# Performance work log

Measured on AMD Instinct MI355X. Metric: run time of the kernel, lower is better.

Reference implementation:

```python
import jax, jax.numpy as jnp
import numpy as np

B, N, H = 128, 512, 512
NEG_INF = -1e30


def setup_inputs() -> dict:
    key = jax.random.key(0)
    k1, k2, k3, k4 = jax.random.split(key, 4)
    code_feat = jax.random.normal(k1, (B, N, H), dtype=jnp.float32)
    node_mask = jax.random.randint(k2, (B, N), 0, 2, dtype=jnp.int32)
    node_mask = node_mask.at[:, 0].set(1)  # ensure >=1 valid node per sample
    scale = 1.0 / np.sqrt(H)
    W_sa = jax.random.normal(k3, (H, H), dtype=jnp.float32) * scale
    b_sa = jnp.zeros((H,), dtype=jnp.float32)
    w_sc = jax.random.normal(k4, (H,), dtype=jnp.float32) * scale
    b_sc = jnp.zeros((), dtype=jnp.float32)
    return {"code_feat": code_feat, "node_mask": node_mask,
            "W_sa": W_sa, "b_sa": b_sa, "w_sc": w_sc, "b_sc": b_sc}


def reference(code_feat, node_mask, W_sa, b_sa, w_sc, b_sc):
    # code_sa_tanh = self_atten_scalar(tanh(self_atten(code_feat)))  -> [B, N]
    h = jnp.tanh(jnp.einsum('bnh,hk->bnk', code_feat, W_sa) + b_sa)
    scores = jnp.einsum('bnk,k->bn', h, w_sc) + b_sc  # [B, N]
    valid = node_mask.astype(bool)
    # masked_select + softmax over selected nodes == masked softmax; invalid
    # positions get weight 0, so the weighted sum over all nodes matches the
    # original per-sample bmm over the ragged selection exactly.
    scores = jnp.where(valid, scores, NEG_INF)
    attn = jax.nn.softmax(scores, axis=1)  # [B, N]
    pooled = jnp.einsum('bn,bnh->bh', attn, code_feat)  # [B, H]
    return jnp.tanh(pooled)
```

## Files before the change

kernel.cpp:

```cpp
#include <hip/hip_runtime.h>

#define NEG_INF (-1e30f)

typedef __bf16 bf16x8 __attribute__((ext_vector_type(8)));
typedef float  f32x4  __attribute__((ext_vector_type(4)));
typedef unsigned short ushort;

__device__ inline ushort f2bf(float f) {
    union { float f; unsigned u; } v; v.f = f;
    unsigned r = v.u + 0x7fffu + ((v.u >> 16) & 1u);
    return (ushort)(r >> 16);
}

__device__ inline float fast_tanhf(float x) {
    return 1.0f - 2.0f / (1.0f + __expf(2.0f * x));
}

__global__ void convw_kernel(const float* __restrict__ W, ushort* __restrict__ Wt) {
    int i = blockIdx.x * 256 + threadIdx.x;
    int h = i >> 9, c = i & 511;
    Wt[c * 512 + h] = f2bf(W[i]);
}

__global__ __launch_bounds__(512) void gemm_scores_kernel(
    const float* __restrict__ feat, const ushort* __restrict__ Wt,
    const float* __restrict__ b_sa, const float* __restrict__ w_sc,
    const float* __restrict__ b_sc, const int* __restrict__ mask,
    float* __restrict__ scores) {

    __shared__ ushort Alds[64 * 40];
    __shared__ ushort Blds[512 * 40];
    __shared__ float  wpart[8][64];

    const int tid  = threadIdx.x;
    const int m0   = blockIdx.x * 64;
    const int lane = tid & 63;
    const int wv   = tid >> 6;
    const int lr   = lane & 15;
    const int lk   = (lane >> 4) * 8;

    f32x4 acc[4][4];
#pragma unroll
    for (int a = 0; a < 4; ++a)
#pragma unroll
        for (int bn = 0; bn < 4; ++bn)
            acc[a][bn] = (f32x4){0.f, 0.f, 0.f, 0.f};

    const int arow = tid >> 3;
    const int acol = (tid & 7) * 4;
    const int brow = tid >> 2;
    const int bcol = (tid & 3) * 8;

    for (int k0 = 0; k0 < 512; k0 += 32) {
        __syncthreads();
        {
            const float4 v = *reinterpret_cast<const float4*>(
                feat + (size_t)(m0 + arow) * 512 + k0 + acol);
            ushort4 bv;
            bv.x = f2bf(v.x); bv.y = f2bf(v.y); bv.z = f2bf(v.z); bv.w = f2bf(v.w);
            *reinterpret_cast<ushort4*>(&Alds[arow * 40 + acol]) = bv;
        }
#pragma unroll
        for (int it = 0; it < 4; ++it) {
            int c = it * 128 + brow;
            uint4 raw = *reinterpret_cast<const uint4*>(Wt + (size_t)c * 512 + k0 + bcol);
            *reinterpret_cast<uint4*>(&Blds[c * 40 + bcol]) = raw;
        }
        __syncthreads();

        bf16x8 af[4], bfv[4];
#pragma unroll
        for (int a = 0; a < 4; ++a)
            af[a] = *reinterpret_cast<const bf16x8*>(&Alds[(a * 16 + lr) * 40 + lk]);
#pragma unroll
        for (int bn = 0; bn < 4; ++bn)
            bfv[bn] = *reinterpret_cast<const bf16x8*>(&Blds[(wv * 64 + bn * 16 + lr) * 40 + lk]);
#pragma unroll
        for (int a = 0; a < 4; ++a)
#pragma unroll
            for (int bn = 0; bn < 4; ++bn)
                acc[a][bn] = __builtin_amdgcn_mfma_f32_16x16x32_bf16(
                    af[a], bfv[bn], acc[a][bn], 0, 0, 0);
    }

    float rsum[4][4];
#pragma unroll
    for (int a = 0; a < 4; ++a)
#pragma unroll
        for (int r = 0; r < 4; ++r) rsum[a][r] = 0.0f;

#pragma unroll
    for (int bn = 0; bn < 4; ++bn) {
        int c = wv * 64 + bn * 16 + lr;
        float wsc = w_sc[c];
        float bsa = b_sa[c];
#pragma unroll
        for (int a = 0; a < 4; ++a)
#pragma unroll
            for (int r = 0; r < 4; ++r)
                rsum[a][r] += fast_tanhf(acc[a][bn][r] + bsa) * wsc;
    }
#pragma unroll
    for (int a = 0; a < 4; ++a)
#pragma unroll
        for (int r = 0; r < 4; ++r) {
            float v = rsum[a][r];
            v += __shfl_xor(v, 1);
            v += __shfl_xor(v, 2);
            v += __shfl_xor(v, 4);
            v += __shfl_xor(v, 8);
            rsum[a][r] = v;
        }
    if (lr == 0) {
        int rg = lane >> 4;
#pragma unroll
        for (int a = 0; a < 4; ++a)
#pragma unroll
            for (int r = 0; r < 4; ++r)
                wpart[wv][a * 16 + rg * 4 + r] = rsum[a][r];
    }
    __syncthreads();
    if (tid < 64) {
        float s = b_sc[0];
#pragma unroll
        for (int w2 = 0; w2 < 8; ++w2) s += wpart[w2][tid];
        int m = m0 + tid;
        scores[m] = mask[m] ? s : NEG_INF;
    }
}

__global__ void softmax_kernel(float* __restrict__ scores) {
    int b = blockIdx.x, t = threadIdx.x;
    float s0 = scores[b * 512 + t];
    float s1 = scores[b * 512 + t + 256];
    float m = fmaxf(s0, s1);
#pragma unroll
    for (int o = 1; o < 64; o <<= 1) m = fmaxf(m, __shfl_xor(m, o));
    __shared__ float red[4];
    if ((t & 63) == 0) red[t >> 6] = m;
    __syncthreads();
    m = fmaxf(fmaxf(red[0], red[1]), fmaxf(red[2], red[3]));
    float e0 = __expf(s0 - m), e1 = __expf(s1 - m);
    float z = e0 + e1;
#pragma unroll
    for (int o = 1; o < 64; o <<= 1) z += __shfl_xor(z, o);
    __syncthreads();
    if ((t & 63) == 0) red[t >> 6] = z;
    __syncthreads();
    float inv = 1.0f / (red[0] + red[1] + red[2] + red[3]);
    scores[b * 512 + t]       = e0 * inv;
    scores[b * 512 + t + 256] = e1 * inv;
}

__global__ void pool_kernel(const float* __restrict__ feat,
                            const float* __restrict__ probs,
                            float* __restrict__ part) {
    int b = blockIdx.x, c = blockIdx.y, t = threadIdx.x;
    __shared__ float pl[64];
    if (t < 64) pl[t] = probs[b * 512 + c * 64 + t];
    __syncthreads();
    const float* fbase = feat + ((size_t)b * 512 + c * 64) * 512;
    float a0 = 0.f, a1 = 0.f;
#pragma unroll 8
    for (int n = 0; n < 64; ++n) {
        float p = pl[n];
        a0 = fmaf(p, fbase[(size_t)n * 512 + t], a0);
        a1 = fmaf(p, fbase[(size_t)n * 512 + t + 256], a1);
    }
    part[(size_t)c * 65536 + b * 512 + t]       = a0;
    part[(size_t)c * 65536 + b * 512 + t + 256] = a1;
}

__global__ void finish_kernel(const float* __restrict__ part, float* __restrict__ out) {
    int i = blockIdx.x * 256 + threadIdx.x;
    float s = 0.f;
#pragma unroll
    for (int c = 0; c < 8; ++c) s += part[(size_t)c * 65536 + i];
    out[i] = fast_tanhf(s);
}

extern "C" void kernel_launch(void* const* d_in, const int* in_sizes, int n_in,
                              void* d_out, int out_size, void* d_ws, size_t ws_size,
                              hipStream_t stream) {
    const float* feat = (const float*)d_in[0];
    const int*   mask = (const int*)d_in[1];
    const float* W_sa = (const float*)d_in[2];
    const float* b_sa = (const float*)d_in[3];
    const float* w_sc = (const float*)d_in[4];
    const float* b_sc = (const float*)d_in[5];
    float* out = (float*)d_out;

    char* ws = (char*)d_ws;
    ushort* Wt    = (ushort*)ws;
    float*  scores = (float*)(ws + 524288);
    float*  part   = (float*)(ws + 524288 + 262144);

    hipLaunchKernelGGL(convw_kernel, dim3(1024), dim3(256), 0, stream, W_sa, Wt);
    hipLaunchKernelGGL(gemm_scores_kernel, dim3(1024), dim3(512), 0, stream,
                       feat, Wt, b_sa, w_sc, b_sc, mask, scores);
    hipLaunchKernelGGL(softmax_kernel, dim3(128), dim3(256), 0, stream, scores);
    hipLaunchKernelGGL(pool_kernel, dim3(128, 8), dim3(256), 0, stream, feat, scores, part);
    hipLaunchKernelGGL(finish_kernel, dim3(256), dim3(256), 0, stream, part, out);
}
```

Before: 96.68 us.

## Retile score GEMM into 128x128 blocks with direct-to-LDS weight loads

The score GEMM moves from 64-row blocks covering all 512 output columns to 128x128 tiles on a 4x512 grid of 256-thread blocks. Weight tiles are copied straight into LDS with global_load_lds, and feature loads are issued before the barrier. Because each block now covers only part of the columns, partial row scores go to a workspace and the softmax kernel sums them and applies the mask and bias. The pool kernel switches to float4 loads over 128-node chunks with an LDS reduction, halving the partial outputs. The trade-off is that each feature tile is now read four times, once per column block, plus extra workspace traffic for the partial scores.

```diff
diff --git a/kernel.cpp b/kernel.cpp
--- a/kernel.cpp
+++ b/kernel.cpp
@@ -6,14 +6,20 @@
 typedef float  f32x4  __attribute__((ext_vector_type(4)));
 typedef unsigned short ushort;
 
-__device__ inline ushort f2bf(float f) {
+__device__ __forceinline__ float fast_tanhf(float x) {
+    return 1.0f - 2.0f / (1.0f + __expf(2.0f * x));
+}
+
+__device__ __forceinline__ ushort f2bf(float f) {
     union { float f; unsigned u; } v; v.f = f;
     unsigned r = v.u + 0x7fffu + ((v.u >> 16) & 1u);
     return (ushort)(r >> 16);
 }
 
-__device__ inline float fast_tanhf(float x) {
-    return 1.0f - 2.0f / (1.0f + __expf(2.0f * x));
+__device__ __forceinline__ void gload_lds16(const void* gsrc, void* ldsdst) {
+    __builtin_amdgcn_global_load_lds(
+        (const __attribute__((address_space(1))) unsigned int*)gsrc,
+        (__attribute__((address_space(3))) unsigned int*)ldsdst, 16, 0, 0);
 }
 
 __global__ void convw_kernel(const float* __restrict__ W, ushort* __restrict__ Wt) {
@@ -22,65 +28,75 @@
     Wt[c * 512 + h] = f2bf(W[i]);
 }
 
-__global__ __launch_bounds__(512) void gemm_scores_kernel(
+__global__ __launch_bounds__(256) void gemm_scores_kernel(
     const float* __restrict__ feat, const ushort* __restrict__ Wt,
     const float* __restrict__ b_sa, const float* __restrict__ w_sc,
-    const float* __restrict__ b_sc, const int* __restrict__ mask,
-    float* __restrict__ scores) {
-
-    __shared__ ushort Alds[64 * 40];
-    __shared__ ushort Blds[512 * 40];
-    __shared__ float  wpart[8][64];
+    float* __restrict__ sp) {
+
+    __shared__ ushort Alds[128 * 40];
+    __shared__ ushort Blds[128 * 32];
+    __shared__ float  redE[4][64];
 
     const int tid  = threadIdx.x;
-    const int m0   = blockIdx.x * 64;
+    const int by   = blockIdx.x;
+    const int m0   = blockIdx.y * 128;
+    const int n0   = by * 128;
     const int lane = tid & 63;
     const int wv   = tid >> 6;
+    const int wm   = wv >> 1, wn = wv & 1;
     const int lr   = lane & 15;
-    const int lk   = (lane >> 4) * 8;
+    const int kg   = lane >> 4;
+    const int lk   = kg * 8;
+
+    const int arow = tid >> 1;
+    const int aseg = (tid & 1) * 16;
+    const float* agp = feat + (size_t)(m0 + arow) * 512 + aseg;
 
     f32x4 acc[4][4];
 #pragma unroll
     for (int a = 0; a < 4; ++a)
 #pragma unroll
-        for (int bn = 0; bn < 4; ++bn)
-            acc[a][bn] = (f32x4){0.f, 0.f, 0.f, 0.f};
-
-    const int arow = tid >> 3;
-    const int acol = (tid & 7) * 4;
-    const int brow = tid >> 2;
-    const int bcol = (tid & 3) * 8;
+        for (int b = 0; b < 4; ++b) acc[a][b] = (f32x4){0.f, 0.f, 0.f, 0.f};
+
+    const int o1 = tid + 256;
+    const ushort* bg0 = Wt + (size_t)(n0 + (tid >> 2)) * 512 + (tid & 3) * 8;
+    const ushort* bg1 = Wt + (size_t)(n0 + (o1 >> 2)) * 512 + (o1 & 3) * 8;
 
     for (int k0 = 0; k0 < 512; k0 += 32) {
+        const float4 v0 = *reinterpret_cast<const float4*>(agp + k0);
+        const float4 v1 = *reinterpret_cast<const float4*>(agp + k0 + 4);
+        const float4 v2 = *reinterpret_cast<const float4*>(agp + k0 + 8);
+        const float4 v3 = *reinterpret_cast<const float4*>(agp + k0 + 12);
+
         __syncthreads();
-        {
-            const float4 v = *reinterpret_cast<const float4*>(
-                feat + (size_t)(m0 + arow) * 512 + k0 + acol);
-            ushort4 bv;
-            bv.x = f2bf(v.x); bv.y = f2bf(v.y); bv.z = f2bf(v.z); bv.w = f2bf(v.w);
-            *reinterpret_cast<ushort4*>(&Alds[arow * 40 + acol]) = bv;
-        }
-#pragma unroll
-        for (int it = 0; it < 4; ++it) {
-            int c = it * 128 + brow;
-            uint4 raw = *reinterpret_cast<const uint4*>(Wt + (size_t)c * 512 + k0 + bcol);
-            *reinterpret_cast<uint4*>(&Blds[c * 40 + bcol]) = raw;
-        }
+
+        gload_lds16(bg0 + k0, (char*)Blds + wv * 1024);
+        gload_lds16(bg1 + k0, (char*)Blds + 4096 + wv * 1024);
+
+        bf16x8 h0, h1;
+        h0[0] = (__bf16)v0.x; h0[1] = (__bf16)v0.y; h0[2] = (__bf16)v0.z; h0[3] = (__bf16)v0.w;
+        h0[4] = (__bf16)v1.x; h0[5] = (__bf16)v1.y; h0[6] = (__bf16)v1.z; h0[7] = (__bf16)v1.w;
+        h1[0] = (__bf16)v2.x; h1[1] = (__bf16)v2.y; h1[2] = (__bf16)v2.z; h1[3] = (__bf16)v2.w;
+        h1[4] = (__bf16)v3.x; h1[5] = (__bf16)v3.y; h1[6] = (__bf16)v3.z; h1[7] = (__bf16)v3.w;
+        *reinterpret_cast<bf16x8*>(&Alds[arow * 40 + aseg]) = h0;
+        *reinterpret_cast<bf16x8*>(&Alds[arow * 40 + aseg + 8]) = h1;
+
         __syncthreads();
 
         bf16x8 af[4], bfv[4];
 #pragma unroll
         for (int a = 0; a < 4; ++a)
-            af[a] = *reinterpret_cast<const bf16x8*>(&Alds[(a * 16 + lr) * 40 + lk]);
-#pragma unroll
-        for (int bn = 0; bn < 4; ++bn)
-            bfv[bn] = *reinterpret_cast<const bf16x8*>(&Blds[(wv * 64 + bn * 16 + lr) * 40 + lk]);
-#pragma unroll
-        for (int a = 0; a < 4; ++a)
-#pragma unroll
-            for (int bn = 0; bn < 4; ++bn)
-                acc[a][bn] = __builtin_amdgcn_mfma_f32_16x16x32_bf16(
-                    af[a], bfv[bn], acc[a][bn], 0, 0, 0);
+            af[a] = *reinterpret_cast<const bf16x8*>(
+                &Alds[(wm * 64 + a * 16 + lr) * 40 + lk]);
+#pragma unroll
+        for (int b = 0; b < 4; ++b)
+            bfv[b] = *reinterpret_cast<const bf16x8*>(&Blds[(wn * 64 + b * 16 + lr) * 32 + lk]);
+#pragma unroll
+        for (int a = 0; a < 4; ++a)
+#pragma unroll
+            for (int b = 0; b < 4; ++b)
+                acc[a][b] = __builtin_amdgcn_mfma_f32_16x16x32_bf16(
+                    af[a], bfv[b], acc[a][b], 0, 0, 0);
     }
 
     float rsum[4][4];
@@ -90,15 +106,15 @@
         for (int r = 0; r < 4; ++r) rsum[a][r] = 0.0f;
 
 #pragma unroll
-    for (int bn = 0; bn < 4; ++bn) {
-        int c = wv * 64 + bn * 16 + lr;
-        float wsc = w_sc[c];
-        float bsa = b_sa[c];
+    for (int b = 0; b < 4; ++b) {
+        int col = n0 + wn * 64 + b * 16 + lr;
+        float wsc = w_sc[col];
+        float bsa = b_sa[col];
 #pragma unroll
         for (int a = 0; a < 4; ++a)
 #pragma unroll
             for (int r = 0; r < 4; ++r)
-                rsum[a][r] += fast_tanhf(acc[a][bn][r] + bsa) * wsc;
+                rsum[a][r] += fast_tanhf(acc[a][b][r] + bsa) * wsc;
     }
 #pragma unroll
     for (int a = 0; a < 4; ++a)
@@ -112,27 +128,27 @@
             rsum[a][r] = v;
         }
     if (lr == 0) {
-        int rg = lane >> 4;
 #pragma unroll
         for (int a = 0; a < 4; ++a)
 #pragma unroll
             for (int r = 0; r < 4; ++r)
-                wpart[wv][a * 16 + rg * 4 + r] = rsum[a][r];
-    }
-    __syncthreads();
-    if (tid < 64) {
-        float s = b_sc[0];
-#pragma unroll
-        for (int w2 = 0; w2 < 8; ++w2) s += wpart[w2][tid];
-        int m = m0 + tid;
-        scores[m] = mask[m] ? s : NEG_INF;
-    }
-}
-
-__global__ void softmax_kernel(float* __restrict__ scores) {
+                redE[wv][a * 16 + kg * 4 + r] = rsum[a][r];
+    }
+    __syncthreads();
+    if (tid < 128) {
+        int wmo = tid >> 6, r64 = tid & 63;
+        sp[(size_t)by * 65536 + m0 + tid] = redE[wmo * 2][r64] + redE[wmo * 2 + 1][r64];
+    }
+}
+
+__global__ void softmax_kernel(const float* __restrict__ sp, const float* __restrict__ b_sc,
+                               const int* __restrict__ mask, float* __restrict__ probs) {
     int b = blockIdx.x, t = threadIdx.x;
-    float s0 = scores[b * 512 + t];
-    float s1 = scores[b * 512 + t + 256];
+    int i0 = b * 512 + t, i1 = i0 + 256;
+    float s0 = sp[i0] + sp[65536 + i0] + sp[131072 + i0] + sp[196608 + i0] + b_sc[0];
+    float s1 = sp[i1] + sp[65536 + i1] + sp[131072 + i1] + sp[196608 + i1] + b_sc[0];
+    if (!mask[i0]) s0 = NEG_INF;
+    if (!mask[i1]) s1 = NEG_INF;
     float m = fmaxf(s0, s1);
 #pragma unroll
     for (int o = 1; o < 64; o <<= 1) m = fmaxf(m, __shfl_xor(m, o));
@@ -148,34 +164,42 @@
     if ((t & 63) == 0) red[t >> 6] = z;
     __syncthreads();
     float inv = 1.0f / (red[0] + red[1] + red[2] + red[3]);
-    scores[b * 512 + t]       = e0 * inv;
-    scores[b * 512 + t + 256] = e1 * inv;
+    probs[i0] = e0 * inv;
+    probs[i1] = e1 * inv;
 }
 
 __global__ void pool_kernel(const float* __restrict__ feat,
                             const float* __restrict__ probs,
                             float* __restrict__ part) {
     int b = blockIdx.x, c = blockIdx.y, t = threadIdx.x;
-    __shared__ float pl[64];
-    if (t < 64) pl[t] = probs[b * 512 + c * 64 + t];
-    __syncthreads();
-    const float* fbase = feat + ((size_t)b * 512 + c * 64) * 512;
-    float a0 = 0.f, a1 = 0.f;
+    __shared__ float pl[128];
+    __shared__ float red2[2][512];
+    if (t < 128) pl[t] = probs[b * 512 + c * 128 + t];
+    __syncthreads();
+    int col4 = (t & 127) * 4;
+    int stripe = t >> 7;
+    const float* fb = feat + ((size_t)(b * 512 + c * 128 + stripe * 64)) * 512 + col4;
+    float4 a4 = {0.f, 0.f, 0.f, 0.f};
 #pragma unroll 8
     for (int n = 0; n < 64; ++n) {
-        float p = pl[n];
-        a0 = fmaf(p, fbase[(size_t)n * 512 + t], a0);
-        a1 = fmaf(p, fbase[(size_t)n * 512 + t + 256], a1);
-    }
-    part[(size_t)c * 65536 + b * 512 + t]       = a0;
-    part[(size_t)c * 65536 + b * 512 + t + 256] = a1;
+        float p = pl[stripe * 64 + n];
+        const float4 f4 = *reinterpret_cast<const float4*>(fb + (size_t)n * 512);
+        a4.x = fmaf(p, f4.x, a4.x);
+        a4.y = fmaf(p, f4.y, a4.y);
+        a4.z = fmaf(p, f4.z, a4.z);
+        a4.w = fmaf(p, f4.w, a4.w);
+    }
+    *reinterpret_cast<float4*>(&red2[stripe][col4]) = a4;
+    __syncthreads();
+    float x0 = red2[0][t] + red2[1][t];
+    float x1 = red2[0][t + 256] + red2[1][t + 256];
+    part[(size_t)c * 65536 + b * 512 + t]       = x0;
+    part[(size_t)c * 65536 + b * 512 + t + 256] = x1;
 }
 
 __global__ void finish_kernel(const float* __restrict__ part, float* __restrict__ out) {
     int i = blockIdx.x * 256 + threadIdx.x;
-    float s = 0.f;
-#pragma unroll
-    for (int c = 0; c < 8; ++c) s += part[(size_t)c * 65536 + i];
+    float s = part[i] + part[65536 + i] + part[131072 + i] + part[196608 + i];
     out[i] = fast_tanhf(s);
 }
 
@@ -192,13 +216,15 @@
 
     char* ws = (char*)d_ws;
     ushort* Wt    = (ushort*)ws;
-    float*  scores = (float*)(ws + 524288);
-    float*  part   = (float*)(ws + 524288 + 262144);
+    float*  sp    = (float*)(ws + (512 << 10));
+    float*  probs = (float*)(ws + (512 << 10) + (1024 << 10));
+    float*  part  = (float*)(ws + (512 << 10) + (1280 << 10));
 
     hipLaunchKernelGGL(convw_kernel, dim3(1024), dim3(256), 0, stream, W_sa, Wt);
-    hipLaunchKernelGGL(gemm_scores_kernel, dim3(1024), dim3(512), 0, stream,
-                       feat, Wt, b_sa, w_sc, b_sc, mask, scores);
-    hipLaunchKernelGGL(softmax_kernel, dim3(128), dim3(256), 0, stream, scores);
-    hipLaunchKernelGGL(pool_kernel, dim3(128, 8), dim3(256), 0, stream, feat, scores, part);
+    hipLaunchKernelGGL(gemm_scores_kernel, dim3(4, 512), dim3(256), 0, stream,
+                       feat, Wt, b_sa, w_sc, sp);
+    hipLaunchKernelGGL(softmax_kernel, dim3(128), dim3(256), 0, stream,
+                       sp, b_sc, mask, probs);
+    hipLaunchKernelGGL(pool_kernel, dim3(128, 4), dim3(256), 0, stream, feat, probs, part);
     hipLaunchKernelGGL(finish_kernel, dim3(256), dim3(256), 0, stream, part, out);
 }
```

Measured after the change: 118.2 us. 22.2% more time.
